# Optimization experiments

Measured on AMD Instinct MI355X. Metric: run time of the kernel, lower is better.

The kernel has to match this reference:

```python
import jax, jax.numpy as jnp
import numpy as np
import math

B, T, D, E, K, H = 2, 2048, 1024, 8, 2, 4096
CAP_F = 1.25
N = B * T
C = math.ceil(CAP_F * N * K / E)  # 1280


def setup_inputs() -> dict:
    key = jax.random.key(0)
    ks = jax.random.split(key, 4)
    s = 0.02
    return {
        "h": jax.random.normal(ks[0], (B, T, D), jnp.float32),
        "Wr": (jax.random.normal(ks[1], (D, E), jnp.float32) * s),
        "br": jnp.zeros((E,), jnp.float32),
        "ln_scale": jnp.ones((E, D), jnp.float32),
        "ln_bias": jnp.zeros((E, D), jnp.float32),
        "W1": (jax.random.normal(ks[2], (E, D, 2 * H), jnp.float32) * s),
        "b1": jnp.zeros((E, 2 * H), jnp.float32),
        "W2": (jax.random.normal(ks[3], (E, H, D), jnp.float32) * s),
        "b2": jnp.zeros((E, D), jnp.float32),
    }


def _cv_squared(x, eps=1e-9):
    m = x.mean()
    v = ((x - m) ** 2).mean()  # biased variance, as torch var(unbiased=False)
    return v / (jnp.maximum(m, eps) ** 2 + eps)


def reference(h, Wr, br, ln_scale, ln_bias, W1, b1, W2, b2):
    x = h.reshape(N, D)
    # ---- router (eval mode: no noise, temperature=1.0) ----
    logits = x @ Wr + br                                   # [N, E]
    z_loss = jnp.mean(logits ** 2) * 1e-4
    probs = jax.nn.softmax(logits, axis=-1)
    importance = probs.sum(0)                              # [E]
    topk_vals, topk_idx = jax.lax.top_k(logits, K)         # [N, K]
    gates = jax.nn.softmax(topk_vals, axis=-1)             # [N, K]

    # ---- capacity-limited positions, pass-major order (pass 0 all tokens, then pass 1) ----
    eid = topk_idx.T.reshape(-1)                           # [K*N] int
    onehot = jax.nn.one_hot(eid, E, dtype=jnp.int32)       # [K*N, E]
    pos = jnp.take_along_axis(jnp.cumsum(onehot, 0) - 1, eid[:, None], axis=1)[:, 0]
    keep = pos < C                                         # [K*N] bool
    load = jnp.sum(onehot * keep[:, None].astype(jnp.int32), axis=0).astype(jnp.float32)
    pos_c = jnp.minimum(pos, C - 1)
    nid = jnp.tile(jnp.arange(N), K)                       # token ids, pass-major

    # normalized combine weights per token (dropped slots get 0)
    keep_nk = keep.reshape(K, N).T                         # [N, K]
    kept_gates = gates * keep_nk.astype(gates.dtype)
    denom = jnp.maximum(kept_gates.sum(1, keepdims=True), 1e-8)
    w_flat = (kept_gates / denom).T.reshape(-1)            # [K*N], pass-major

    # ---- dispatch: scatter tokens into [E, C, D] (== einsum('nec,nd->ecd')) ----
    keep_f = keep[:, None].astype(x.dtype)
    expert_in = jnp.zeros((E, C, D), x.dtype).at[eid, pos_c].add(x[nid] * keep_f)

    # ---- experts: PreNorm + GLU FFN (dropout off in eval) ----
    mu = expert_in.mean(-1, keepdims=True)
    var = ((expert_in - mu) ** 2).mean(-1, keepdims=True)
    xn = (expert_in - mu) / jnp.sqrt(var + 1e-5)
    xn = xn * ln_scale[:, None, :] + ln_bias[:, None, :]
    u = jnp.einsum('ecd,edh->ech', xn, W1) + b1[:, None, :]  # [E, C, 2H]
    a, g = u[..., :H], u[..., H:]
    v = a * jax.nn.sigmoid(g)                               # GLU(dim=-1)
    expert_out = jnp.einsum('ech,ehd->ecd', v, W2) + b2[:, None, :]

    # ---- combine: gather expert slots, weight, scatter-add to tokens ----
    gathered = expert_out[eid, pos_c] * w_flat[:, None]
    y = jnp.zeros((N, D), x.dtype).at[nid].add(gathered).reshape(B, T, D)

    balance_loss = 0.5 * (_cv_squared(importance) + _cv_squared(load))
    return y, balance_loss, z_loss
```

## Files before the change

### kernel.cpp

```cpp
#include <hip/hip_runtime.h>
#include <cstdint>
#include <cstddef>

#define N_TOK 4096
#define DIM   1024
#define NEXP  8
#define HID   4096
#define TWO_H 8192
#define CAP   1280

typedef __bf16 bf16x8 __attribute__((ext_vector_type(8)));
typedef float  f32x4  __attribute__((ext_vector_type(4)));

__device__ __forceinline__ unsigned short f2bf(float f) {
  union { float f; unsigned u; } v; v.f = f;
  unsigned r = v.u + 0x7FFF + ((v.u >> 16) & 1);
  return (unsigned short)(r >> 16);
}
__device__ __forceinline__ float bf2f(unsigned short b) {
  union { unsigned u; float f; } v; v.u = ((unsigned)b) << 16;
  return v.f;
}

__device__ __forceinline__ void gll16(const unsigned short* g, unsigned short* l) {
  __builtin_amdgcn_global_load_lds(
      (const __attribute__((address_space(1))) uint32_t*)g,
      (__attribute__((address_space(3))) uint32_t*)l, 16, 0, 0);
}

__global__ void k_zero(float* imp, float* zsum) {
  if (threadIdx.x < NEXP) imp[threadIdx.x] = 0.f;
  if (threadIdx.x == 0) zsum[0] = 0.f;
}

__global__ void k_conv_w1(const float* __restrict__ W1, unsigned short* __restrict__ W1t) {
  __shared__ float tA[32][33];
  __shared__ float tG[32][33];
  int h0 = blockIdx.x * 32, d0 = blockIdx.y * 32, e = blockIdx.z;
  int tx = threadIdx.x & 31, ty = threadIdx.x >> 5;
  const float* src = W1 + (size_t)e * DIM * TWO_H;
  for (int i = 0; i < 32; i += 8) {
    int d = d0 + ty + i;
    tA[ty + i][tx] = src[(size_t)d * TWO_H + h0 + tx];
    tG[ty + i][tx] = src[(size_t)d * TWO_H + HID + h0 + tx];
  }
  __syncthreads();
  unsigned short* dst = W1t + (size_t)e * TWO_H * DIM;
  for (int i = 0; i < 64; i += 8) {
    int r = ty + i;
    int hh = r >> 1, p = r & 1;
    float v = p ? tG[tx][hh] : tA[tx][hh];
    dst[(size_t)(2 * h0 + r) * DIM + d0 + tx] = f2bf(v);
  }
}

__global__ void k_conv_w2(const float* __restrict__ W2, unsigned short* __restrict__ W2t) {
  __shared__ float t[32][33];
  int d0 = blockIdx.x * 32, h0 = blockIdx.y * 32, e = blockIdx.z;
  int tx = threadIdx.x & 31, ty = threadIdx.x >> 5;
  const float* src = W2 + (size_t)e * HID * DIM;
  for (int i = 0; i < 32; i += 8)
    t[ty + i][tx] = src[(size_t)(h0 + ty + i) * DIM + d0 + tx];
  __syncthreads();
  unsigned short* dst = W2t + (size_t)e * DIM * HID;
  for (int i = 0; i < 32; i += 8)
    dst[(size_t)(d0 + ty + i) * HID + h0 + tx] = f2bf(t[tx][ty + i]);
}

__global__ void k_pack_b1(const float* __restrict__ b1, float* __restrict__ b1p) {
  int g = blockIdx.x * blockDim.x + threadIdx.x;
  int e = g >> 13, r = g & (TWO_H - 1);
  int h = r >> 1, p = r & 1;
  b1p[g] = b1[e * TWO_H + p * HID + h];
}

__global__ void __launch_bounds__(256) k_router(
    const float* __restrict__ x, const float* __restrict__ Wr, const float* __restrict__ br,
    int* __restrict__ idx, float* __restrict__ gate,
    float* __restrict__ imp, float* __restrict__ zsum) {
  __shared__ float sW[TWO_H];
  __shared__ float sX[16 * 1028];
  __shared__ float sLG[16 * 8];
  __shared__ float sImp[8];
  __shared__ float sZ;
  int tid = threadIdx.x;
  if (tid < 8) sImp[tid] = 0.f;
  if (tid == 8) sZ = 0.f;
  for (int i = 0; i < 8; ++i) {
    int g = tid + i * 256;
    *(float4*)&sW[g * 4] = *(const float4*)&Wr[g * 4];
  }
  int t0 = blockIdx.x * 16;
  const float* xb = x + (size_t)t0 * DIM;
  for (int i = 0; i < 16; ++i) {
    int g = tid + i * 256;
    int row = g >> 8, c = (g & 255) * 4;
    *(float4*)&sX[row * 1028 + c] = *(const float4*)&xb[(size_t)g * 4];
  }
  __syncthreads();
  int t = tid >> 4, e = (tid >> 1) & 7, half = tid & 1;
  const float* xr = &sX[t * 1028 + half * 512];
  float s = 0.f;
  for (int k = 0; k < 512; k += 4) {
    float4 xv = *(const float4*)&xr[k];
    int kb = (half * 512 + k) * 8 + e;
    s += xv.x * sW[kb] + xv.y * sW[kb + 8] + xv.z * sW[kb + 16] + xv.w * sW[kb + 24];
  }
  s += __shfl_xor(s, 1);
  if (half == 0) sLG[t * 8 + e] = s + br[e];
  __syncthreads();
  if (tid < 16) {
    int n = t0 + tid;
    float lg[8];
    for (int i = 0; i < 8; ++i) lg[i] = sLG[tid * 8 + i];
    float mx = lg[0];
    for (int i = 1; i < 8; ++i) mx = fmaxf(mx, lg[i]);
    float ex[8], den = 0.f, zs = 0.f;
    for (int i = 0; i < 8; ++i) { ex[i] = __expf(lg[i] - mx); den += ex[i]; zs += lg[i] * lg[i]; }
    atomicAdd(&sZ, zs);
    float rden = 1.f / den;
    for (int i = 0; i < 8; ++i) atomicAdd(&sImp[i], ex[i] * rden);
    int i1 = 0;
    for (int i = 1; i < 8; ++i) if (lg[i] > lg[i1]) i1 = i;
    int i2 = -1;
    for (int i = 0; i < 8; ++i) { if (i == i1) continue; if (i2 < 0 || lg[i] > lg[i2]) i2 = i; }
    float e2 = __expf(lg[i2] - lg[i1]);
    float g1 = 1.f / (1.f + e2);
    idx[n * 2] = i1; idx[n * 2 + 1] = i2;
    gate[n * 2] = g1; gate[n * 2 + 1] = 1.f - g1;
  }
  __syncthreads();
  if (tid < 8) atomicAdd(&imp[tid], sImp[tid]);
  if (tid == 8) atomicAdd(zsum, sZ);
}

__global__ void k_scan(const int* __restrict__ idx, int* __restrict__ pos, int* __restrict__ cnt) {
  int wave = threadIdx.x >> 6, lane = threadIdx.x & 63;
  int base = 0;
  for (int c = 0; c < (2 * N_TOK) / 64; ++c) {
    int s = c * 64 + lane;
    int n = s & (N_TOK - 1), k = s >> 12;
    int e = idx[n * 2 + k];
    unsigned long long m = __ballot(e == wave);
    if (e == wave) pos[s] = base + __popcll(m & ((1ull << lane) - 1ull));
    base += __popcll(m);
  }
  if (lane == 0) cnt[wave] = base;
}

__global__ void k_weights(const float* __restrict__ gate, const int* __restrict__ pos,
                          float* __restrict__ wn) {
  int n = blockIdx.x * blockDim.x + threadIdx.x;
  if (n >= N_TOK) return;
  float g0 = gate[n * 2], g1 = gate[n * 2 + 1];
  float k0 = (pos[n] < CAP) ? g0 : 0.f;
  float k1 = (pos[N_TOK + n] < CAP) ? g1 : 0.f;
  float den = fmaxf(k0 + k1, 1e-8f);
  wn[n * 2] = k0 / den; wn[n * 2 + 1] = k1 / den;
}

__global__ void __launch_bounds__(256) k_gather_ln(
    const float* __restrict__ x, const float* __restrict__ lns, const float* __restrict__ lnb,
    const int* __restrict__ idx, const int* __restrict__ pos, unsigned short* __restrict__ Xn) {
  int s = blockIdx.x;
  int p = pos[s];
  if (p >= CAP) return;
  int n = s & (N_TOK - 1), k = s >> 12;
  int e = idx[n * 2 + k];
  const float* xr = x + (size_t)n * DIM;
  int tid = threadIdx.x;
  float v[4], sum = 0.f, sq = 0.f;
  for (int i = 0; i < 4; ++i) { v[i] = xr[tid + i * 256]; sum += v[i]; sq += v[i] * v[i]; }
  for (int o = 32; o > 0; o >>= 1) { sum += __shfl_down(sum, o); sq += __shfl_down(sq, o); }
  __shared__ float ws[8];
  int wv = tid >> 6, ln = tid & 63;
  if (ln == 0) { ws[wv] = sum; ws[4 + wv] = sq; }
  __syncthreads();
  sum = ws[0] + ws[1] + ws[2] + ws[3];
  sq  = ws[4] + ws[5] + ws[6] + ws[7];
  float mu = sum * (1.f / DIM);
  float var = sq * (1.f / DIM) - mu * mu;
  float rs = rsqrtf(var + 1e-5f);
  unsigned short* orow = Xn + ((size_t)e * CAP + p) * DIM;
  const float* sc = lns + (size_t)e * DIM;
  const float* bi = lnb + (size_t)e * DIM;
  for (int i = 0; i < 4; ++i) {
    int d = tid + i * 256;
    orow[d] = f2bf((v[i] - mu) * rs * sc[d] + bi[d]);
  }
}

template<bool GLU, int M_, int N_, int K_>
__global__ void __launch_bounds__(512, 2) k_gemm(
    const unsigned short* __restrict__ A,
    const unsigned short* __restrict__ B,
    const float* __restrict__ bias,
    unsigned short* __restrict__ Cout) {
  constexpr int KT = K_ / 64;
  __shared__ __align__(16) unsigned short smem[65536];

  constexpr int gx = M_ / 256, gy = N_ / 256;
  constexpr int nwg = gx * gy * NEXP;
  int bid = blockIdx.x + gx * (blockIdx.y + gy * blockIdx.z);
  int lid = (bid & 7) * (nwg >> 3) + (bid >> 3);
  int bm = lid % gx; int rest = lid / gx;
  int e  = rest / gy;
  int m0 = bm * 256, n0 = (rest % gy) * 256;

  const unsigned short* Ae = A + (size_t)e * M_ * K_;
  const unsigned short* Be = B + (size_t)e * N_ * K_;
  int tid = threadIdx.x, lane = tid & 63, wave = tid >> 6;
  int wm = wave >> 2, wn = wave & 3;
  int quad = lane >> 4, l16 = lane & 15;

  f32x4 acc[8][4];
#pragma unroll
  for (int i = 0; i < 8; ++i)
#pragma unroll
    for (int j = 0; j < 4; ++j) acc[i][j] = f32x4{0.f, 0.f, 0.f, 0.f};

  int ch = (tid & 3) ^ ((tid >> 3) & 3);
  const unsigned short* Ag0 = Ae + (size_t)(m0 + (tid >> 2)) * K_ + ch * 8;
  const unsigned short* Bg0 = Be + (size_t)(n0 + (tid >> 2)) * K_ + ch * 8;
  unsigned short* sw = smem + wave * 512;

#define STG(gp, bofs, ks, kh) do {                                   \
    int q_ = (2 * (ks) + (kh)) & 3;                                  \
    int kc_ = (ks) < KT ? (ks) : KT - 1;                             \
    size_t ko_ = (size_t)(kc_ * 64 + (kh) * 32);                     \
    gll16(gp + ko_, sw + (bofs) + q_ * 8192);                        \
    gll16(gp + (size_t)128 * K_ + ko_, sw + (bofs) + q_ * 8192 + 4096); \
  } while (0)

  int chR = quad ^ ((l16 >> 1) & 3);
  const unsigned short* rdA = smem + (wm * 128 + l16) * 32 + chR * 8;
  const unsigned short* rdB = smem + 32768 + (wn * 64 + l16) * 32 + chR * 8;

  bf16x8 aF[4], bF[4];
#define LDB(q) { _Pragma("unroll") for (int nf = 0; nf < 4; ++nf) \
    bF[nf] = *(const bf16x8*)(rdB + (q) * 8192 + nf * 512); }
#define LDA(q, h) { _Pragma("unroll") for (int mf = 0; mf < 4; ++mf) \
    aF[mf] = *(const bf16x8*)(rdA + (q) * 8192 + ((h) * 4 + mf) * 512); }
#define MM(h) { _Pragma("unroll") for (int mf = 0; mf < 4; ++mf) \
    _Pragma("unroll") for (int nf = 0; nf < 4; ++nf) \
    acc[(h)*4+mf][nf] = __builtin_amdgcn_mfma_f32_16x16x32_bf16(aF[mf], bF[nf], acc[(h)*4+mf][nf], 0, 0, 0); }
#define WAIT_LGKM0 { asm volatile("s_waitcnt lgkmcnt(0)" ::: "memory"); __builtin_amdgcn_sched_barrier(0); }
#define WAIT_VM4   { asm volatile("s_waitcnt vmcnt(4)"   ::: "memory"); __builtin_amdgcn_sched_barrier(0); }

  STG(Ag0, 0, 0, 0); STG(Bg0, 32768, 0, 0);
  STG(Ag0, 0, 0, 1); STG(Bg0, 32768, 0, 1);
  STG(Ag0, 0, 1, 0); STG(Bg0, 32768, 1, 0);
  asm volatile("s_waitcnt vmcnt(8)" ::: "memory");
  __builtin_amdgcn_sched_barrier(0);
  __builtin_amdgcn_s_barrier();

  for (int kt = 0; kt < KT; ++kt) {
    int q0 = (2 * kt) & 3, q1 = (2 * kt + 1) & 3;
    LDB(q0); LDA(q0, 0);
    STG(Ag0, 0, kt + 1, 1);
    __builtin_amdgcn_s_barrier();
    WAIT_LGKM0;
    __builtin_amdgcn_s_setprio(1); MM(0); __builtin_amdgcn_s_setprio(0);
    __builtin_amdgcn_s_barrier();
    LDA(q0, 1);
    STG(Bg0, 32768, kt + 1, 1);
    WAIT_VM4;
    __builtin_amdgcn_s_barrier();
    WAIT_LGKM0;
    __builtin_amdgcn_s_setprio(1); MM(1); __builtin_amdgcn_s_setprio(0);
    __builtin_amdgcn_s_barrier();
    LDB(q1); LDA(q1, 0);
    STG(Ag0, 0, kt + 2, 0);
    __builtin_amdgcn_s_barrier();
    WAIT_LGKM0;
    __builtin_amdgcn_s_setprio(1); MM(0); __builtin_amdgcn_s_setprio(0);
    __builtin_amdgcn_s_barrier();
    LDA(q1, 1);
    STG(Bg0, 32768, kt + 2, 0);
    WAIT_VM4;
    __builtin_amdgcn_s_barrier();
    WAIT_LGKM0;
    __builtin_amdgcn_s_setprio(1); MM(1); __builtin_amdgcn_s_setprio(0);
    __builtin_amdgcn_s_barrier();
  }
  asm volatile("s_waitcnt vmcnt(0)" ::: "memory");
  __builtin_amdgcn_sched_barrier(0);
  __builtin_amdgcn_s_barrier();

  if (GLU) {
    const float* bp = bias + (size_t)e * TWO_H;
    unsigned short* Ce = Cout + (size_t)e * M_ * (N_ >> 1);
#pragma unroll
    for (int mf = 0; mf < 8; ++mf)
#pragma unroll
      for (int nf = 0; nf < 4; ++nf) {
        int pn = n0 + wn * 64 + nf * 16 + l16;
        float b = bp[pn];
#pragma unroll
        for (int r = 0; r < 4; ++r) {
          int row = wm * 128 + mf * 16 + quad * 4 + r;
          float u = acc[mf][nf][r] + b;
          float g = __shfl_xor(u, 1);
          if ((l16 & 1) == 0) {
            float vv = u / (1.f + __expf(-g));
            smem[row * 136 + ((wn * 64 + nf * 16 + l16) >> 1)] = f2bf(vv);
          }
        }
      }
    __syncthreads();
    int c = tid & 15, row0 = tid >> 4;
    for (int p = 0; p < 8; ++p) {
      int row = row0 + p * 32;
      *(int4*)&Ce[(size_t)(m0 + row) * (N_ >> 1) + (n0 >> 1) + c * 8] =
          *(const int4*)&smem[row * 136 + c * 8];
    }
  } else {
    unsigned short* Ce = Cout + (size_t)e * M_ * N_;
    for (int h = 0; h < 2; ++h) {
      if (h) __syncthreads();
#pragma unroll
      for (int mf2 = 0; mf2 < 4; ++mf2)
#pragma unroll
        for (int nf = 0; nf < 4; ++nf) {
          int mf = 4 * h + mf2;
          int col = wn * 64 + nf * 16 + l16;
          int lr = wm * 64 + mf2 * 16 + quad * 4;
#pragma unroll
          for (int r = 0; r < 4; ++r)
            smem[(lr + r) * 264 + col] = f2bf(acc[mf][nf][r]);
        }
      __syncthreads();
      int c = tid & 31, row0 = tid >> 5;
      for (int p = 0; p < 8; ++p) {
        int row = row0 + p * 16;
        int grow = m0 + (row >> 6) * 128 + h * 64 + (row & 63);
        *(int4*)&Ce[(size_t)grow * N_ + n0 + c * 8] =
            *(const int4*)&smem[row * 264 + c * 8];
      }
    }
  }
#undef STG
#undef LDB
#undef LDA
#undef MM
#undef WAIT_LGKM0
#undef WAIT_VM4
}

__global__ void __launch_bounds__(256) k_gather_out(
    const unsigned short* __restrict__ Yexp, const float* __restrict__ b2,
    const int* __restrict__ idx, const int* __restrict__ pos,
    const float* __restrict__ wn, float* __restrict__ y) {
  int n = blockIdx.x, tid = threadIdx.x;
  int e0 = idx[n * 2], e1 = idx[n * 2 + 1];
  int p0 = min(pos[n], CAP - 1), p1 = min(pos[N_TOK + n], CAP - 1);
  float w0 = wn[n * 2], w1 = wn[n * 2 + 1];
  const unsigned short* r0 = Yexp + ((size_t)e0 * CAP + p0) * DIM;
  const unsigned short* r1 = Yexp + ((size_t)e1 * CAP + p1) * DIM;
  const float* bb0 = b2 + (size_t)e0 * DIM;
  const float* bb1 = b2 + (size_t)e1 * DIM;
  float* yr = y + (size_t)n * DIM;
  for (int i = 0; i < 4; ++i) {
    int d = tid + i * 256;
    yr[d] = w0 * (bf2f(r0[d]) + bb0[d]) + w1 * (bf2f(r1[d]) + bb1[d]);
  }
}

__global__ void k_losses(const float* __restrict__ imp, const int* __restrict__ cnt,
                         const float* __restrict__ zsum, float* __restrict__ out) {
  if (threadIdx.x != 0 || blockIdx.x != 0) return;
  double li[8], ll[8], mi = 0.0, ml = 0.0;
  for (int i = 0; i < 8; ++i) {
    li[i] = imp[i];
    ll[i] = (double)min(cnt[i], CAP);
    mi += li[i]; ml += ll[i];
  }
  mi /= 8.0; ml /= 8.0;
  double vi = 0.0, vl = 0.0;
  for (int i = 0; i < 8; ++i) { vi += (li[i] - mi) * (li[i] - mi); vl += (ll[i] - ml) * (ll[i] - ml); }
  vi /= 8.0; vl /= 8.0;
  const double eps = 1e-9;
  double cvi = vi / (fmax(mi, eps) * fmax(mi, eps) + eps);
  double cvl = vl / (fmax(ml, eps) * fmax(ml, eps) + eps);
  out[0] = (float)(0.5 * (cvi + cvl));
  out[1] = (float)((double)zsum[0] / (double)(N_TOK * NEXP) * 1e-4);
}

extern "C" void kernel_launch(void* const* d_in, const int* in_sizes, int n_in,
                              void* d_out, int out_size, void* d_ws, size_t ws_size,
                              hipStream_t stream) {
  const float* h   = (const float*)d_in[0];
  const float* Wr  = (const float*)d_in[1];
  const float* br  = (const float*)d_in[2];
  const float* lns = (const float*)d_in[3];
  const float* lnb = (const float*)d_in[4];
  const float* W1  = (const float*)d_in[5];
  const float* b1  = (const float*)d_in[6];
  const float* W2  = (const float*)d_in[7];
  const float* b2  = (const float*)d_in[8];
  float* out = (float*)d_out;

  char* ws = (char*)d_ws;
  size_t off = 0;
  auto alloc = [&](size_t bytes) { char* p = ws + off; off += (bytes + 255) & ~(size_t)255; return p; };
  unsigned short* W1t = (unsigned short*)alloc((size_t)NEXP * TWO_H * DIM * 2);
  unsigned short* W2t = (unsigned short*)alloc((size_t)NEXP * DIM * HID * 2);
  unsigned short* Xn  = (unsigned short*)alloc((size_t)NEXP * CAP * DIM * 2);
  unsigned short* V   = (unsigned short*)alloc((size_t)NEXP * CAP * HID * 2);
  unsigned short* Yx  = (unsigned short*)alloc((size_t)NEXP * CAP * DIM * 2);
  float* b1p  = (float*)alloc((size_t)NEXP * TWO_H * 4);
  int*   idx  = (int*)alloc((size_t)N_TOK * 2 * 4);
  float* gate = (float*)alloc((size_t)N_TOK * 2 * 4);
  float* wn   = (float*)alloc((size_t)N_TOK * 2 * 4);
  int*   pos  = (int*)alloc((size_t)2 * N_TOK * 4);
  int*   cnt  = (int*)alloc(64);
  float* imp  = (float*)alloc(64);
  float* zsum = (float*)alloc(64);
  (void)ws_size; (void)in_sizes; (void)n_in; (void)out_size;

  k_zero<<<dim3(1), dim3(64), 0, stream>>>(imp, zsum);
  k_conv_w1<<<dim3(HID / 32, DIM / 32, NEXP), dim3(256), 0, stream>>>(W1, W1t);
  k_conv_w2<<<dim3(DIM / 32, HID / 32, NEXP), dim3(256), 0, stream>>>(W2, W2t);
  k_pack_b1<<<dim3(NEXP * TWO_H / 256), dim3(256), 0, stream>>>(b1, b1p);
  k_router<<<dim3(N_TOK / 16), dim3(256), 0, stream>>>(h, Wr, br, idx, gate, imp, zsum);
  k_scan<<<dim3(1), dim3(512), 0, stream>>>(idx, pos, cnt);
  k_weights<<<dim3(16), dim3(256), 0, stream>>>(gate, pos, wn);
  k_gather_ln<<<dim3(2 * N_TOK), dim3(256), 0, stream>>>(h, lns, lnb, idx, pos, Xn);
  k_gemm<true, CAP, TWO_H, DIM><<<dim3(CAP / 256, TWO_H / 256, NEXP), dim3(512), 0, stream>>>(
      Xn, W1t, b1p, V);
  k_gemm<false, CAP, DIM, HID><<<dim3(CAP / 256, DIM / 256, NEXP), dim3(512), 0, stream>>>(
      V, W2t, b1p, Yx);
  k_gather_out<<<dim3(N_TOK), dim3(256), 0, stream>>>(Yx, b2, idx, pos, wn, out);
  k_losses<<<dim3(1), dim3(64), 0, stream>>>(imp, cnt, zsum, out + (size_t)N_TOK * DIM);
}
```

Before: 889.3 us.

## Vectorize weight conversion, LN gather and combine; stage scan indices in LDS; loosen vmcnt wait

The weight transpose and convert kernels now use 64x64 tiles with float4 loads and 16-byte packed bf16 stores. The LayerNorm gather and the output combine kernels switch to float4 and ushort4 vector accesses. The single-block scan first copies the routing indices into shared memory. The GEMM pipeline waits at vmcnt(6) instead of vmcnt(4), letting more global-to-LDS loads stay in flight, and the templated GEMM is split into two named kernel wrappers. Together these aim to cut memory-transaction overhead in the bandwidth-bound helper kernels. The looser wait relies on the STG ordering to stay correct.

```diff
diff --git a/kernel.cpp b/kernel.cpp
--- a/kernel.cpp
+++ b/kernel.cpp
@@ -33,38 +33,54 @@
   if (threadIdx.x == 0) zsum[0] = 0.f;
 }
 
-__global__ void k_conv_w1(const float* __restrict__ W1, unsigned short* __restrict__ W1t) {
-  __shared__ float tA[32][33];
-  __shared__ float tG[32][33];
-  int h0 = blockIdx.x * 32, d0 = blockIdx.y * 32, e = blockIdx.z;
-  int tx = threadIdx.x & 31, ty = threadIdx.x >> 5;
+__global__ void __launch_bounds__(256) k_conv_w1(const float* __restrict__ W1,
+                                                 unsigned short* __restrict__ W1t) {
+  __shared__ float tP[2][64][65];
+  int h0 = blockIdx.x * 64, d0 = blockIdx.y * 64, e = blockIdx.z;
+  int tid = threadIdx.x;
   const float* src = W1 + (size_t)e * DIM * TWO_H;
-  for (int i = 0; i < 32; i += 8) {
-    int d = d0 + ty + i;
-    tA[ty + i][tx] = src[(size_t)d * TWO_H + h0 + tx];
-    tG[ty + i][tx] = src[(size_t)d * TWO_H + HID + h0 + tx];
+  for (int i = 0; i < 4; ++i) {
+    int g = tid + i * 256;
+    int dd = g >> 4, c = g & 15;
+    float4 a = *(const float4*)&src[(size_t)(d0 + dd) * TWO_H + h0 + c * 4];
+    float4 gg = *(const float4*)&src[(size_t)(d0 + dd) * TWO_H + HID + h0 + c * 4];
+    *(float4*)&tP[0][dd][c * 4] = a;
+    *(float4*)&tP[1][dd][c * 4] = gg;
   }
   __syncthreads();
   unsigned short* dst = W1t + (size_t)e * TWO_H * DIM;
-  for (int i = 0; i < 64; i += 8) {
-    int r = ty + i;
+  for (int i = 0; i < 4; ++i) {
+    int o = tid + i * 256;
+    int r = o >> 3, cc = o & 7;
     int hh = r >> 1, p = r & 1;
-    float v = p ? tG[tx][hh] : tA[tx][hh];
-    dst[(size_t)(2 * h0 + r) * DIM + d0 + tx] = f2bf(v);
-  }
-}
-
-__global__ void k_conv_w2(const float* __restrict__ W2, unsigned short* __restrict__ W2t) {
-  __shared__ float t[32][33];
-  int d0 = blockIdx.x * 32, h0 = blockIdx.y * 32, e = blockIdx.z;
-  int tx = threadIdx.x & 31, ty = threadIdx.x >> 5;
+    unsigned short pk[8];
+#pragma unroll
+    for (int j = 0; j < 8; ++j) pk[j] = f2bf(tP[p][cc * 8 + j][hh]);
+    *(int4*)&dst[(size_t)(2 * h0 + r) * DIM + d0 + cc * 8] = *(const int4*)pk;
+  }
+}
+
+__global__ void __launch_bounds__(256) k_conv_w2(const float* __restrict__ W2,
+                                                 unsigned short* __restrict__ W2t) {
+  __shared__ float t[64][65];
+  int h0 = blockIdx.x * 64, d0 = blockIdx.y * 64, e = blockIdx.z;
+  int tid = threadIdx.x;
   const float* src = W2 + (size_t)e * HID * DIM;
-  for (int i = 0; i < 32; i += 8)
-    t[ty + i][tx] = src[(size_t)(h0 + ty + i) * DIM + d0 + tx];
+  for (int i = 0; i < 4; ++i) {
+    int g = tid + i * 256;
+    int hh = g >> 4, c = g & 15;
+    *(float4*)&t[hh][c * 4] = *(const float4*)&src[(size_t)(h0 + hh) * DIM + d0 + c * 4];
+  }
   __syncthreads();
   unsigned short* dst = W2t + (size_t)e * DIM * HID;
-  for (int i = 0; i < 32; i += 8)
-    dst[(size_t)(d0 + ty + i) * HID + h0 + tx] = f2bf(t[tx][ty + i]);
+  for (int i = 0; i < 2; ++i) {
+    int o = tid + i * 256;
+    int rd = o >> 3, cc = o & 7;
+    unsigned short pk[8];
+#pragma unroll
+    for (int j = 0; j < 8; ++j) pk[j] = f2bf(t[cc * 8 + j][rd]);
+    *(int4*)&dst[(size_t)(d0 + rd) * HID + h0 + cc * 8] = *(const int4*)pk;
+  }
 }
 
 __global__ void k_pack_b1(const float* __restrict__ b1, float* __restrict__ b1p) {
@@ -135,12 +151,17 @@
 }
 
 __global__ void k_scan(const int* __restrict__ idx, int* __restrict__ pos, int* __restrict__ cnt) {
-  int wave = threadIdx.x >> 6, lane = threadIdx.x & 63;
+  __shared__ int sIdx[2 * N_TOK];
+  int tid = threadIdx.x;
+  for (int i = 0; i < 4; ++i)
+    ((int4*)sIdx)[tid + i * 512] = ((const int4*)idx)[tid + i * 512];
+  __syncthreads();
+  int wave = tid >> 6, lane = tid & 63;
   int base = 0;
   for (int c = 0; c < (2 * N_TOK) / 64; ++c) {
     int s = c * 64 + lane;
     int n = s & (N_TOK - 1), k = s >> 12;
-    int e = idx[n * 2 + k];
+    int e = sIdx[n * 2 + k];
     unsigned long long m = __ballot(e == wave);
     if (e == wave) pos[s] = base + __popcll(m & ((1ull << lane) - 1ull));
     base += __popcll(m);
@@ -169,8 +190,9 @@
   int e = idx[n * 2 + k];
   const float* xr = x + (size_t)n * DIM;
   int tid = threadIdx.x;
-  float v[4], sum = 0.f, sq = 0.f;
-  for (int i = 0; i < 4; ++i) { v[i] = xr[tid + i * 256]; sum += v[i]; sq += v[i] * v[i]; }
+  float4 v = *(const float4*)&xr[tid * 4];
+  float sum = v.x + v.y + v.z + v.w;
+  float sq  = v.x * v.x + v.y * v.y + v.z * v.z + v.w * v.w;
   for (int o = 32; o > 0; o >>= 1) { sum += __shfl_down(sum, o); sq += __shfl_down(sq, o); }
   __shared__ float ws[8];
   int wv = tid >> 6, ln = tid & 63;
@@ -184,21 +206,22 @@
   unsigned short* orow = Xn + ((size_t)e * CAP + p) * DIM;
   const float* sc = lns + (size_t)e * DIM;
   const float* bi = lnb + (size_t)e * DIM;
-  for (int i = 0; i < 4; ++i) {
-    int d = tid + i * 256;
-    orow[d] = f2bf((v[i] - mu) * rs * sc[d] + bi[d]);
-  }
+  float4 s4 = *(const float4*)&sc[tid * 4];
+  float4 b4 = *(const float4*)&bi[tid * 4];
+  unsigned short o4[4];
+  o4[0] = f2bf((v.x - mu) * rs * s4.x + b4.x);
+  o4[1] = f2bf((v.y - mu) * rs * s4.y + b4.y);
+  o4[2] = f2bf((v.z - mu) * rs * s4.z + b4.z);
+  o4[3] = f2bf((v.w - mu) * rs * s4.w + b4.w);
+  *(uint2*)&orow[tid * 4] = *(const uint2*)o4;
 }
 
 template<bool GLU, int M_, int N_, int K_>
-__global__ void __launch_bounds__(512, 2) k_gemm(
-    const unsigned short* __restrict__ A,
-    const unsigned short* __restrict__ B,
-    const float* __restrict__ bias,
-    unsigned short* __restrict__ Cout) {
+__device__ __forceinline__ void gemm_body(
+    const unsigned short* __restrict__ A, const unsigned short* __restrict__ B,
+    const float* __restrict__ bias, unsigned short* __restrict__ Cout,
+    unsigned short* smem) {
   constexpr int KT = K_ / 64;
-  __shared__ __align__(16) unsigned short smem[65536];
-
   constexpr int gx = M_ / 256, gy = N_ / 256;
   constexpr int nwg = gx * gy * NEXP;
   int bid = blockIdx.x + gx * (blockIdx.y + gy * blockIdx.z);
@@ -245,7 +268,7 @@
     _Pragma("unroll") for (int nf = 0; nf < 4; ++nf) \
     acc[(h)*4+mf][nf] = __builtin_amdgcn_mfma_f32_16x16x32_bf16(aF[mf], bF[nf], acc[(h)*4+mf][nf], 0, 0, 0); }
 #define WAIT_LGKM0 { asm volatile("s_waitcnt lgkmcnt(0)" ::: "memory"); __builtin_amdgcn_sched_barrier(0); }
-#define WAIT_VM4   { asm volatile("s_waitcnt vmcnt(4)"   ::: "memory"); __builtin_amdgcn_sched_barrier(0); }
+#define WAIT_VM6   { asm volatile("s_waitcnt vmcnt(6)"   ::: "memory"); __builtin_amdgcn_sched_barrier(0); }
 
   STG(Ag0, 0, 0, 0); STG(Bg0, 32768, 0, 0);
   STG(Ag0, 0, 0, 1); STG(Bg0, 32768, 0, 1);
@@ -264,7 +287,7 @@
     __builtin_amdgcn_s_barrier();
     LDA(q0, 1);
     STG(Bg0, 32768, kt + 1, 1);
-    WAIT_VM4;
+    WAIT_VM6;
     __builtin_amdgcn_s_barrier();
     WAIT_LGKM0;
     __builtin_amdgcn_s_setprio(1); MM(1); __builtin_amdgcn_s_setprio(0);
@@ -277,7 +300,7 @@
     __builtin_amdgcn_s_barrier();
     LDA(q1, 1);
     STG(Bg0, 32768, kt + 2, 0);
-    WAIT_VM4;
+    WAIT_VM6;
     __builtin_amdgcn_s_barrier();
     WAIT_LGKM0;
     __builtin_amdgcn_s_setprio(1); MM(1); __builtin_amdgcn_s_setprio(0);
@@ -344,7 +367,20 @@
 #undef LDA
 #undef MM
 #undef WAIT_LGKM0
-#undef WAIT_VM4
+#undef WAIT_VM6
+}
+
+__global__ void __launch_bounds__(512, 2) k_gemm1(
+    const unsigned short* __restrict__ A, const unsigned short* __restrict__ B,
+    const float* __restrict__ bias, unsigned short* __restrict__ Cout) {
+  __shared__ __align__(16) unsigned short smem[65536];
+  gemm_body<true, CAP, TWO_H, DIM>(A, B, bias, Cout, smem);
+}
+__global__ void __launch_bounds__(512, 2) k_gemm2(
+    const unsigned short* __restrict__ A, const unsigned short* __restrict__ B,
+    const float* __restrict__ bias, unsigned short* __restrict__ Cout) {
+  __shared__ __align__(16) unsigned short smem[65536];
+  gemm_body<false, CAP, DIM, HID>(A, B, bias, Cout, smem);
 }
 
 __global__ void __launch_bounds__(256) k_gather_out(
@@ -360,10 +396,17 @@
   const float* bb0 = b2 + (size_t)e0 * DIM;
   const float* bb1 = b2 + (size_t)e1 * DIM;
   float* yr = y + (size_t)n * DIM;
-  for (int i = 0; i < 4; ++i) {
-    int d = tid + i * 256;
-    yr[d] = w0 * (bf2f(r0[d]) + bb0[d]) + w1 * (bf2f(r1[d]) + bb1[d]);
-  }
+  int d4 = tid * 4;
+  ushort4 a0 = *(const ushort4*)&r0[d4];
+  ushort4 a1 = *(const ushort4*)&r1[d4];
+  float4 b0 = *(const float4*)&bb0[d4];
+  float4 b1 = *(const float4*)&bb1[d4];
+  float4 o;
+  o.x = w0 * (bf2f(a0.x) + b0.x) + w1 * (bf2f(a1.x) + b1.x);
+  o.y = w0 * (bf2f(a0.y) + b0.y) + w1 * (bf2f(a1.y) + b1.y);
+  o.z = w0 * (bf2f(a0.z) + b0.z) + w1 * (bf2f(a1.z) + b1.z);
+  o.w = w0 * (bf2f(a0.w) + b0.w) + w1 * (bf2f(a1.w) + b1.w);
+  *(float4*)&yr[d4] = o;
 }
 
 __global__ void k_losses(const float* __restrict__ imp, const int* __restrict__ cnt,
@@ -419,17 +462,15 @@
   (void)ws_size; (void)in_sizes; (void)n_in; (void)out_size;
 
   k_zero<<<dim3(1), dim3(64), 0, stream>>>(imp, zsum);
-  k_conv_w1<<<dim3(HID / 32, DIM / 32, NEXP), dim3(256), 0, stream>>>(W1, W1t);
-  k_conv_w2<<<dim3(DIM / 32, HID / 32, NEXP), dim3(256), 0, stream>>>(W2, W2t);
+  k_conv_w1<<<dim3(HID / 64, DIM / 64, NEXP), dim3(256), 0, stream>>>(W1, W1t);
+  k_conv_w2<<<dim3(HID / 64, DIM / 64, NEXP), dim3(256), 0, stream>>>(W2, W2t);
   k_pack_b1<<<dim3(NEXP * TWO_H / 256), dim3(256), 0, stream>>>(b1, b1p);
   k_router<<<dim3(N_TOK / 16), dim3(256), 0, stream>>>(h, Wr, br, idx, gate, imp, zsum);
   k_scan<<<dim3(1), dim3(512), 0, stream>>>(idx, pos, cnt);
   k_weights<<<dim3(16), dim3(256), 0, stream>>>(gate, pos, wn);
   k_gather_ln<<<dim3(2 * N_TOK), dim3(256), 0, stream>>>(h, lns, lnb, idx, pos, Xn);
-  k_gemm<true, CAP, TWO_H, DIM><<<dim3(CAP / 256, TWO_H / 256, NEXP), dim3(512), 0, stream>>>(
-      Xn, W1t, b1p, V);
-  k_gemm<false, CAP, DIM, HID><<<dim3(CAP / 256, DIM / 256, NEXP), dim3(512), 0, stream>>>(
-      V, W2t, b1p, Yx);
+  k_gemm1<<<dim3(CAP / 256, TWO_H / 256, NEXP), dim3(512), 0, stream>>>(Xn, W1t, b1p, V);
+  k_gemm2<<<dim3(CAP / 256, DIM / 256, NEXP), dim3(512), 0, stream>>>(V, W2t, b1p, Yx);
   k_gather_out<<<dim3(N_TOK), dim3(256), 0, stream>>>(Yx, b2, idx, pos, wn, out);
   k_losses<<<dim3(1), dim3(64), 0, stream>>>(imp, cnt, zsum, out + (size_t)N_TOK * DIM);
 }
```

After: 875.0 us. About the same (-1.6%).
